# Kernel optimization log

Measured on AMD Instinct MI355X. Metric: run time of the kernel, lower is better.

The kernel has to match this reference:

```python
import jax, jax.numpy as jnp
import numpy as np

LN_EPS = 1e-3  # keras LayerNormalization default epsilon


def setup_inputs() -> dict:
    key = jax.random.key(0)
    ks = jax.random.split(key, 4)
    B, F, DIN = 1024, 128, 64
    H, D = 8, 64
    x = jax.random.normal(ks[0], (B, F, DIN), dtype=jnp.float32)
    query_w = jax.random.normal(ks[1], (DIN, H, D), dtype=jnp.float32) * 0.05
    key_w = jax.random.normal(ks[2], (DIN, H, D), dtype=jnp.float32) * 0.05
    res_w = jax.random.normal(ks[3], (DIN, H, D), dtype=jnp.float32) * 0.05
    ln_gamma = jnp.ones((D,), dtype=jnp.float32)
    ln_beta = jnp.zeros((D,), dtype=jnp.float32)
    return {"x": x, "query_w": query_w, "key_w": key_w, "res_w": res_w,
            "ln_gamma": ln_gamma, "ln_beta": ln_beta}


def _layer_norm(x, gamma, beta):
    mu = jnp.mean(x, axis=-1, keepdims=True)
    var = jnp.mean(jnp.square(x - mu), axis=-1, keepdims=True)
    return (x - mu) * jax.lax.rsqrt(var + LN_EPS) * gamma + beta


def reference(x, query_w, key_w, res_w, ln_gamma, ln_beta):
    # x: [B,F,DIN]; weights: [DIN,H,D]; projections -> [H,B,F,D]
    q = jnp.einsum('bfi,ihd->hbfd', x, query_w)
    k = jnp.einsum('bfi,ihd->hbfd', x, key_w)
    v = jnp.einsum('bfi,ihd->hbfd', x, key_w)  # faithful to source bug: v uses key_w
    D = q.shape[-1]
    scores = jnp.einsum('hbfd,hbgd->hbfg', q, k) / jnp.sqrt(jnp.float32(D))
    attn = jax.nn.sigmoid(scores)          # sigmoid, not softmax
    atten_v = jnp.einsum('hbfg,hbgd->hbfd', attn, v)
    res = jnp.einsum('bfi,ihd->hbfd', x, res_w)
    atten_v = _layer_norm(atten_v, ln_gamma, ln_beta)
    return (atten_v, res)
```

## Files before the change

kernel.cpp:

```cpp
#include <hip/hip_runtime.h>
#include <hip/hip_bf16.h>

typedef __bf16 bf16;
typedef bf16 bf16x4 __attribute__((ext_vector_type(4)));
typedef bf16 bf16x8 __attribute__((ext_vector_type(8)));
typedef float f32x4 __attribute__((ext_vector_type(4)));

#define XS_OFF   0
#define WQ_OFF   9216
#define WK_OFF   13824
#define WR_OFF   18432
#define Q_OFF    23040
#define KRM_OFF  9216
#define KCM_OFF  0
#define AT_OFF   18432
#define RS64     72
#define RS128    136

__device__ inline short f2bs(float v) { bf16 b = (bf16)v; return __builtin_bit_cast(short, b); }
__device__ inline bf16x8 ldfrag(const short* s) {
  uint4 u = *(const uint4*)s;
  return __builtin_bit_cast(bf16x8, u);
}
__device__ inline f32x4 mfma16(bf16x8 a, bf16x8 b, f32x4 c) {
  return __builtin_amdgcn_mfma_f32_16x16x32_bf16(a, b, c, 0, 0, 0);
}

__global__ __launch_bounds__(256) void fused_mha_kernel(
    const float* __restrict__ x, const float* __restrict__ qw,
    const float* __restrict__ kw, const float* __restrict__ rw,
    const float* __restrict__ gamma, const float* __restrict__ beta,
    float* __restrict__ out)
{
  __shared__ __align__(16) short smem[32256];

  const int bx   = blockIdx.x;
  const int h    = bx >> 10;
  const int b    = bx & 1023;
  const int tid  = threadIdx.x;
  const int w    = tid >> 6;
  const int lane = tid & 63;
  const int q    = lane >> 4;
  const int l15  = lane & 15;

  {
    const float4* xg = (const float4*)(x + (size_t)b * 8192);
    for (int r = 0; r < 8; ++r) {
      int idx4 = r * 256 + tid;
      float4 v = xg[idx4];
      int f = idx4 >> 4;
      int i = (idx4 & 15) * 4;
      bf16x4 t;
      t[0] = (bf16)v.x; t[1] = (bf16)v.y; t[2] = (bf16)v.z; t[3] = (bf16)v.w;
      *(bf16x4*)(void*)&smem[XS_OFF + f * RS64 + i] = t;
    }
    const float* wsrc[3] = {qw, kw, rw};
    const int   woff[3] = {WQ_OFF, WK_OFF, WR_OFF};
    int wi = tid >> 2;
    int dg = (tid & 3) * 16;
    for (int s = 0; s < 3; ++s) {
      const float* base = wsrc[s] + (size_t)wi * 512 + h * 64 + dg;
      short* dst = smem + woff[s];
      for (int u = 0; u < 4; ++u) {
        float4 v = *(const float4*)(base + u * 4);
        int d0 = dg + u * 4;
        dst[(d0 + 0) * RS64 + wi] = f2bs(v.x);
        dst[(d0 + 1) * RS64 + wi] = f2bs(v.y);
        dst[(d0 + 2) * RS64 + wi] = f2bs(v.z);
        dst[(d0 + 3) * RS64 + wi] = f2bs(v.w);
      }
    }
  }
  __syncthreads();

  f32x4 acc[8];
  auto proj = [&](int wt) {
    for (int t = 0; t < 8; ++t) acc[t] = (f32x4){0.f, 0.f, 0.f, 0.f};
    for (int ks = 0; ks < 2; ++ks) {
      int ke = ks * 32 + q * 8;
      bf16x8 a0 = ldfrag(smem + XS_OFF + ((2 * w + 0) * 16 + l15) * RS64 + ke);
      bf16x8 a1 = ldfrag(smem + XS_OFF + ((2 * w + 1) * 16 + l15) * RS64 + ke);
      for (int nt = 0; nt < 4; ++nt) {
        bf16x8 bb = ldfrag(smem + wt + (nt * 16 + l15) * RS64 + ke);
        acc[nt]     = mfma16(a0, bb, acc[nt]);
        acc[4 + nt] = mfma16(a1, bb, acc[4 + nt]);
      }
    }
  };

  proj(WR_OFF);
  {
    float* outR = out + 67108864 + (size_t)bx * 8192;
    for (int t = 0; t < 8; ++t) {
      int mt2 = t >> 2, nt = t & 3;
      int row0 = (2 * w + mt2) * 16 + q * 4;
      int col  = nt * 16 + l15;
      for (int r = 0; r < 4; ++r) outR[(row0 + r) * 64 + col] = acc[t][r];
    }
  }

  proj(WQ_OFF);
  for (int t = 0; t < 8; ++t) {
    int mt2 = t >> 2, nt = t & 3;
    int row0 = (2 * w + mt2) * 16 + q * 4;
    int col  = nt * 16 + l15;
    for (int r = 0; r < 4; ++r) smem[Q_OFF + (row0 + r) * RS64 + col] = f2bs(acc[t][r]);
  }

  proj(WK_OFF);
  __syncthreads();
  for (int t = 0; t < 8; ++t) {
    int mt2 = t >> 2, nt = t & 3;
    int row0 = (2 * w + mt2) * 16 + q * 4;
    int col  = nt * 16 + l15;
    for (int r = 0; r < 4; ++r) {
      short kb = f2bs(acc[t][r]);
      smem[KRM_OFF + (row0 + r) * RS64 + col]  = kb;
      smem[KCM_OFF + col * RS128 + (row0 + r)] = kb;
    }
  }
  __syncthreads();

  float gam[4], bet[4];
  for (int j = 0; j < 4; ++j) { gam[j] = gamma[j * 16 + l15]; bet[j] = beta[j * 16 + l15]; }

  float* out0 = out + (size_t)bx * 8192;
  for (int c = 0; c < 4; ++c) {
    f32x4 sacc[4];
    for (int j = 0; j < 4; ++j) sacc[j] = (f32x4){0.f, 0.f, 0.f, 0.f};
    int mtg = 2 * c + (w & 1);
    int ntb = (w >> 1) * 4;
    for (int ks = 0; ks < 2; ++ks) {
      int ke = ks * 32 + q * 8;
      bf16x8 aS = ldfrag(smem + Q_OFF + (mtg * 16 + l15) * RS64 + ke);
      for (int j = 0; j < 4; ++j) {
        bf16x8 bS = ldfrag(smem + KRM_OFF + ((ntb + j) * 16 + l15) * RS64 + ke);
        sacc[j] = mfma16(aS, bS, sacc[j]);
      }
    }
    int rowA0 = (w & 1) * 16 + q * 4;
    for (int j = 0; j < 4; ++j)
      for (int r = 0; r < 4; ++r) {
        float s = sacc[j][r] * 0.125f;
        float a = 1.0f / (1.0f + __expf(-s));
        smem[AT_OFF + (rowA0 + r) * RS128 + (ntb + j) * 16 + l15] = f2bs(a);
      }
    __syncthreads();

    if (w < 2) {
      f32x4 oacc[4];
      for (int j = 0; j < 4; ++j) oacc[j] = (f32x4){0.f, 0.f, 0.f, 0.f};
      for (int ks = 0; ks < 4; ++ks) {
        int ke = ks * 32 + q * 8;
        bf16x8 aO = ldfrag(smem + AT_OFF + (w * 16 + l15) * RS128 + ke);
        for (int j = 0; j < 4; ++j) {
          bf16x8 bO = ldfrag(smem + KCM_OFF + (j * 16 + l15) * RS128 + ke);
          oacc[j] = mfma16(aO, bO, oacc[j]);
        }
      }
      for (int r = 0; r < 4; ++r) {
        float v0 = oacc[0][r], v1 = oacc[1][r], v2 = oacc[2][r], v3 = oacc[3][r];
        float s1 = v0 + v1 + v2 + v3;
        float s2 = v0 * v0 + v1 * v1 + v2 * v2 + v3 * v3;
        s1 += __shfl_xor(s1, 1);  s2 += __shfl_xor(s2, 1);
        s1 += __shfl_xor(s1, 2);  s2 += __shfl_xor(s2, 2);
        s1 += __shfl_xor(s1, 4);  s2 += __shfl_xor(s2, 4);
        s1 += __shfl_xor(s1, 8);  s2 += __shfl_xor(s2, 8);
        float mean = s1 * 0.015625f;
        float var  = s2 * 0.015625f - mean * mean;
        float rstd = rsqrtf(var + 1e-3f);
        int gf = c * 32 + w * 16 + q * 4 + r;
        float* dst = out0 + gf * 64 + l15;
        dst[0]  = (v0 - mean) * rstd * gam[0] + bet[0];
        dst[16] = (v1 - mean) * rstd * gam[1] + bet[1];
        dst[32] = (v2 - mean) * rstd * gam[2] + bet[2];
        dst[48] = (v3 - mean) * rstd * gam[3] + bet[3];
      }
    }
    __syncthreads();
  }
}

extern "C" void kernel_launch(void* const* d_in, const int* in_sizes, int n_in,
                              void* d_out, int out_size, void* d_ws, size_t ws_size,
                              hipStream_t stream) {
  const float* x     = (const float*)d_in[0];
  const float* qw    = (const float*)d_in[1];
  const float* kw    = (const float*)d_in[2];
  const float* rw    = (const float*)d_in[3];
  const float* gamma = (const float*)d_in[4];
  const float* beta  = (const float*)d_in[5];
  float* out = (float*)d_out;
  fused_mha_kernel<<<dim3(8192), dim3(256), 0, stream>>>(x, qw, kw, rw, gamma, beta, out);
}
```

Measured before the change: 674.5 us.

## Swizzle LDS layout, shrink shared memory, and give each wave independent attention rows

Replaces the padded shared-memory rows with XOR-swizzled unpadded layouts and reuses regions, cutting LDS from about 63KB to 48KB per block so more blocks fit per CU (launch bounds hint 3). Each wave now owns 32 query rows and computes scores, sigmoid, the AV product and LayerNorm for them in a private scratch area. This removes the per-chunk block barriers and the idle half of the waves in the old AV stage. It also keeps Q fragments in registers and uses a fast reciprocal for the sigmoid, which raises register pressure and slightly changes rounding.

```diff
diff --git a/kernel.cpp b/kernel.cpp
--- a/kernel.cpp
+++ b/kernel.cpp
@@ -7,15 +7,9 @@
 typedef float f32x4 __attribute__((ext_vector_type(4)));
 
 #define XS_OFF   0
-#define WQ_OFF   9216
-#define WK_OFF   13824
-#define WR_OFF   18432
-#define Q_OFF    23040
-#define KRM_OFF  9216
-#define KCM_OFF  0
-#define AT_OFF   18432
-#define RS64     72
-#define RS128    136
+#define W_OFF    8192
+#define SCR_OFF  8192
+#define KCM_OFF  16384
 
 __device__ inline short f2bs(float v) { bf16 b = (bf16)v; return __builtin_bit_cast(short, b); }
 __device__ inline bf16x8 ldfrag(const short* s) {
@@ -26,13 +20,13 @@
   return __builtin_amdgcn_mfma_f32_16x16x32_bf16(a, b, c, 0, 0, 0);
 }
 
-__global__ __launch_bounds__(256) void fused_mha_kernel(
+__global__ __launch_bounds__(256, 3) void fused_mha_kernel(
     const float* __restrict__ x, const float* __restrict__ qw,
     const float* __restrict__ kw, const float* __restrict__ rw,
     const float* __restrict__ gamma, const float* __restrict__ beta,
     float* __restrict__ out)
 {
-  __shared__ __align__(16) short smem[32256];
+  __shared__ __align__(16) short smem[24576];
 
   const int bx   = blockIdx.x;
   const int h    = bx >> 10;
@@ -42,9 +36,12 @@
   const int lane = tid & 63;
   const int q    = lane >> 4;
   const int l15  = lane & 15;
+  const int fr0  = w * 32;
+  const int swl  = (l15 & 7) << 3;
 
   {
     const float4* xg = (const float4*)(x + (size_t)b * 8192);
+#pragma unroll
     for (int r = 0; r < 8; ++r) {
       int idx4 = r * 256 + tid;
       float4 v = xg[idx4];
@@ -52,132 +49,165 @@
       int i = (idx4 & 15) * 4;
       bf16x4 t;
       t[0] = (bf16)v.x; t[1] = (bf16)v.y; t[2] = (bf16)v.z; t[3] = (bf16)v.w;
-      *(bf16x4*)(void*)&smem[XS_OFF + f * RS64 + i] = t;
-    }
-    const float* wsrc[3] = {qw, kw, rw};
-    const int   woff[3] = {WQ_OFF, WK_OFF, WR_OFF};
+      *(bf16x4*)(void*)&smem[XS_OFF + ((f * 64 + i) ^ ((f & 7) << 3))] = t;
+    }
+    const float* wsrc[3] = {rw, qw, kw};
     int wi = tid >> 2;
     int dg = (tid & 3) * 16;
+#pragma unroll
     for (int s = 0; s < 3; ++s) {
       const float* base = wsrc[s] + (size_t)wi * 512 + h * 64 + dg;
-      short* dst = smem + woff[s];
+      short* dst = smem + W_OFF + s * 4096;
+#pragma unroll
       for (int u = 0; u < 4; ++u) {
         float4 v = *(const float4*)(base + u * 4);
         int d0 = dg + u * 4;
-        dst[(d0 + 0) * RS64 + wi] = f2bs(v.x);
-        dst[(d0 + 1) * RS64 + wi] = f2bs(v.y);
-        dst[(d0 + 2) * RS64 + wi] = f2bs(v.z);
-        dst[(d0 + 3) * RS64 + wi] = f2bs(v.w);
+        dst[((d0 + 0) * 64 + wi) ^ (((d0 + 0) & 7) << 3)] = f2bs(v.x);
+        dst[((d0 + 1) * 64 + wi) ^ (((d0 + 1) & 7) << 3)] = f2bs(v.y);
+        dst[((d0 + 2) * 64 + wi) ^ (((d0 + 2) & 7) << 3)] = f2bs(v.z);
+        dst[((d0 + 3) * 64 + wi) ^ (((d0 + 3) & 7) << 3)] = f2bs(v.w);
       }
     }
   }
   __syncthreads();
 
-  f32x4 acc[8];
-  auto proj = [&](int wt) {
+  auto proj = [&](int woff, f32x4* acc) {
+#pragma unroll
     for (int t = 0; t < 8; ++t) acc[t] = (f32x4){0.f, 0.f, 0.f, 0.f};
+#pragma unroll
     for (int ks = 0; ks < 2; ++ks) {
       int ke = ks * 32 + q * 8;
-      bf16x8 a0 = ldfrag(smem + XS_OFF + ((2 * w + 0) * 16 + l15) * RS64 + ke);
-      bf16x8 a1 = ldfrag(smem + XS_OFF + ((2 * w + 1) * 16 + l15) * RS64 + ke);
+      bf16x8 a0 = ldfrag(&smem[XS_OFF + (((fr0 +      l15) * 64 + ke) ^ swl)]);
+      bf16x8 a1 = ldfrag(&smem[XS_OFF + (((fr0 + 16 + l15) * 64 + ke) ^ swl)]);
+#pragma unroll
       for (int nt = 0; nt < 4; ++nt) {
-        bf16x8 bb = ldfrag(smem + wt + (nt * 16 + l15) * RS64 + ke);
+        bf16x8 bb = ldfrag(&smem[woff + (((nt * 16 + l15) * 64 + ke) ^ swl)]);
         acc[nt]     = mfma16(a0, bb, acc[nt]);
         acc[4 + nt] = mfma16(a1, bb, acc[4 + nt]);
       }
     }
   };
 
-  proj(WR_OFF);
   {
+    f32x4 racc[8];
+    proj(W_OFF, racc);
     float* outR = out + 67108864 + (size_t)bx * 8192;
+#pragma unroll
     for (int t = 0; t < 8; ++t) {
-      int mt2 = t >> 2, nt = t & 3;
-      int row0 = (2 * w + mt2) * 16 + q * 4;
+      int mt = t >> 2, nt = t & 3;
+      int row0 = fr0 + mt * 16 + q * 4;
       int col  = nt * 16 + l15;
-      for (int r = 0; r < 4; ++r) outR[(row0 + r) * 64 + col] = acc[t][r];
-    }
-  }
-
-  proj(WQ_OFF);
+#pragma unroll
+      for (int r = 0; r < 4; ++r) outR[(row0 + r) * 64 + col] = racc[t][r];
+    }
+  }
+
+  f32x4 qacc[8]; proj(W_OFF + 4096, qacc);
+  f32x4 kacc[8]; proj(W_OFF + 8192, kacc);
+  __syncthreads();
+
+  short* scr = smem + SCR_OFF + w * 2048;
+
+  {
+#pragma unroll
+    for (int t = 0; t < 8; ++t) {
+      int mt = t >> 2, nt = t & 3;
+      int fro = mt * 16 + q * 4;
+      int col = nt * 16 + l15;
+#pragma unroll
+      for (int r = 0; r < 4; ++r)
+        scr[((fro + r) * 64 + col) ^ (((fro + r) & 7) << 3)] = f2bs(qacc[t][r]);
+    }
+  }
+#pragma unroll
   for (int t = 0; t < 8; ++t) {
-    int mt2 = t >> 2, nt = t & 3;
-    int row0 = (2 * w + mt2) * 16 + q * 4;
-    int col  = nt * 16 + l15;
-    for (int r = 0; r < 4; ++r) smem[Q_OFF + (row0 + r) * RS64 + col] = f2bs(acc[t][r]);
-  }
-
-  proj(WK_OFF);
+    int mt = t >> 2, nt = t & 3;
+    int g0 = fr0 + mt * 16 + q * 4;
+    int d  = nt * 16 + l15;
+#pragma unroll
+    for (int r = 0; r < 4; ++r) {
+      int g = g0 + r;
+      short kb = f2bs(kacc[t][r]);
+      smem[XS_OFF  + ((g * 64  + d) ^ ((g & 7) << 3))] = kb;
+      smem[KCM_OFF + ((d * 128 + g) ^ ((d & 7) << 3))] = kb;
+    }
+  }
+  asm volatile("s_waitcnt lgkmcnt(0)" ::: "memory");
+  __builtin_amdgcn_sched_barrier(0);
+  bf16x8 qf[2][2];
+#pragma unroll
+  for (int mt = 0; mt < 2; ++mt)
+#pragma unroll
+    for (int ks = 0; ks < 2; ++ks)
+      qf[mt][ks] = ldfrag(&scr[((mt * 16 + l15) * 64 + ks * 32 + q * 8) ^ swl]);
+
+  float gam[4], bet[4];
+#pragma unroll
+  for (int j = 0; j < 4; ++j) { gam[j] = gamma[j * 16 + l15]; bet[j] = beta[j * 16 + l15]; }
+
   __syncthreads();
-  for (int t = 0; t < 8; ++t) {
-    int mt2 = t >> 2, nt = t & 3;
-    int row0 = (2 * w + mt2) * 16 + q * 4;
-    int col  = nt * 16 + l15;
-    for (int r = 0; r < 4; ++r) {
-      short kb = f2bs(acc[t][r]);
-      smem[KRM_OFF + (row0 + r) * RS64 + col]  = kb;
-      smem[KCM_OFF + col * RS128 + (row0 + r)] = kb;
-    }
-  }
-  __syncthreads();
-
-  float gam[4], bet[4];
-  for (int j = 0; j < 4; ++j) { gam[j] = gamma[j * 16 + l15]; bet[j] = beta[j * 16 + l15]; }
 
   float* out0 = out + (size_t)bx * 8192;
-  for (int c = 0; c < 4; ++c) {
-    f32x4 sacc[4];
-    for (int j = 0; j < 4; ++j) sacc[j] = (f32x4){0.f, 0.f, 0.f, 0.f};
-    int mtg = 2 * c + (w & 1);
-    int ntb = (w >> 1) * 4;
+#pragma unroll
+  for (int c2 = 0; c2 < 2; ++c2) {
+    f32x4 sacc[8];
+#pragma unroll
+    for (int j = 0; j < 8; ++j) sacc[j] = (f32x4){0.f, 0.f, 0.f, 0.f};
+#pragma unroll
     for (int ks = 0; ks < 2; ++ks) {
       int ke = ks * 32 + q * 8;
-      bf16x8 aS = ldfrag(smem + Q_OFF + (mtg * 16 + l15) * RS64 + ke);
+      bf16x8 aS = qf[c2][ks];
+#pragma unroll
+      for (int nt = 0; nt < 8; ++nt) {
+        bf16x8 bS = ldfrag(&smem[XS_OFF + (((nt * 16 + l15) * 64 + ke) ^ swl)]);
+        sacc[nt] = mfma16(aS, bS, sacc[nt]);
+      }
+    }
+#pragma unroll
+    for (int nt = 0; nt < 8; ++nt) {
+      int gcol = nt * 16 + l15;
+#pragma unroll
+      for (int r = 0; r < 4; ++r) {
+        int fa = q * 4 + r;
+        float e = __expf(-0.125f * sacc[nt][r]);
+        float a = __builtin_amdgcn_rcpf(1.0f + e);
+        scr[((fa * 128 + gcol) ^ ((fa & 7) << 3))] = f2bs(a);
+      }
+    }
+    asm volatile("s_waitcnt lgkmcnt(0)" ::: "memory");
+    __builtin_amdgcn_sched_barrier(0);
+    f32x4 oacc[4];
+#pragma unroll
+    for (int j = 0; j < 4; ++j) oacc[j] = (f32x4){0.f, 0.f, 0.f, 0.f};
+#pragma unroll
+    for (int ks = 0; ks < 4; ++ks) {
+      int ke = ks * 32 + q * 8;
+      bf16x8 aO = ldfrag(&scr[((l15 * 128 + ke) ^ swl)]);
+#pragma unroll
       for (int j = 0; j < 4; ++j) {
-        bf16x8 bS = ldfrag(smem + KRM_OFF + ((ntb + j) * 16 + l15) * RS64 + ke);
-        sacc[j] = mfma16(aS, bS, sacc[j]);
-      }
-    }
-    int rowA0 = (w & 1) * 16 + q * 4;
-    for (int j = 0; j < 4; ++j)
-      for (int r = 0; r < 4; ++r) {
-        float s = sacc[j][r] * 0.125f;
-        float a = 1.0f / (1.0f + __expf(-s));
-        smem[AT_OFF + (rowA0 + r) * RS128 + (ntb + j) * 16 + l15] = f2bs(a);
-      }
-    __syncthreads();
-
-    if (w < 2) {
-      f32x4 oacc[4];
-      for (int j = 0; j < 4; ++j) oacc[j] = (f32x4){0.f, 0.f, 0.f, 0.f};
-      for (int ks = 0; ks < 4; ++ks) {
-        int ke = ks * 32 + q * 8;
-        bf16x8 aO = ldfrag(smem + AT_OFF + (w * 16 + l15) * RS128 + ke);
-        for (int j = 0; j < 4; ++j) {
-          bf16x8 bO = ldfrag(smem + KCM_OFF + (j * 16 + l15) * RS128 + ke);
-          oacc[j] = mfma16(aO, bO, oacc[j]);
-        }
-      }
-      for (int r = 0; r < 4; ++r) {
-        float v0 = oacc[0][r], v1 = oacc[1][r], v2 = oacc[2][r], v3 = oacc[3][r];
-        float s1 = v0 + v1 + v2 + v3;
-        float s2 = v0 * v0 + v1 * v1 + v2 * v2 + v3 * v3;
-        s1 += __shfl_xor(s1, 1);  s2 += __shfl_xor(s2, 1);
-        s1 += __shfl_xor(s1, 2);  s2 += __shfl_xor(s2, 2);
-        s1 += __shfl_xor(s1, 4);  s2 += __shfl_xor(s2, 4);
-        s1 += __shfl_xor(s1, 8);  s2 += __shfl_xor(s2, 8);
-        float mean = s1 * 0.015625f;
-        float var  = s2 * 0.015625f - mean * mean;
-        float rstd = rsqrtf(var + 1e-3f);
-        int gf = c * 32 + w * 16 + q * 4 + r;
-        float* dst = out0 + gf * 64 + l15;
-        dst[0]  = (v0 - mean) * rstd * gam[0] + bet[0];
-        dst[16] = (v1 - mean) * rstd * gam[1] + bet[1];
-        dst[32] = (v2 - mean) * rstd * gam[2] + bet[2];
-        dst[48] = (v3 - mean) * rstd * gam[3] + bet[3];
-      }
-    }
-    __syncthreads();
+        bf16x8 bO = ldfrag(&smem[KCM_OFF + (((j * 16 + l15) * 128 + ke) ^ swl)]);
+        oacc[j] = mfma16(aO, bO, oacc[j]);
+      }
+    }
+#pragma unroll
+    for (int r = 0; r < 4; ++r) {
+      float v0 = oacc[0][r], v1 = oacc[1][r], v2 = oacc[2][r], v3 = oacc[3][r];
+      float s1 = v0 + v1 + v2 + v3;
+      float s2 = v0 * v0 + v1 * v1 + v2 * v2 + v3 * v3;
+      s1 += __shfl_xor(s1, 1);  s2 += __shfl_xor(s2, 1);
+      s1 += __shfl_xor(s1, 2);  s2 += __shfl_xor(s2, 2);
+      s1 += __shfl_xor(s1, 4);  s2 += __shfl_xor(s2, 4);
+      s1 += __shfl_xor(s1, 8);  s2 += __shfl_xor(s2, 8);
+      float mean = s1 * 0.015625f;
+      float var  = s2 * 0.015625f - mean * mean;
+      float rstd = rsqrtf(var + 1e-3f);
+      int gf = fr0 + c2 * 16 + q * 4 + r;
+      float* dst = out0 + gf * 64 + l15;
+      dst[0]  = (v0 - mean) * rstd * gam[0] + bet[0];
+      dst[16] = (v1 - mean) * rstd * gam[1] + bet[1];
+      dst[32] = (v2 - mean) * rstd * gam[2] + bet[2];
+      dst[48] = (v3 - mean) * rstd * gam[3] + bet[3];
+    }
   }
 }
 
```

After: 603.2 us. 10.6% less time.
